# Optimization experiments

Measured on AMD Instinct MI355X. Metric: run time of the kernel, lower is better.

## Reference

```python
import jax, jax.numpy as jnp
import numpy as np

B = 512    # batch
C = 64     # total categorical columns (32 admission + 32 discharge)
N = 32     # graph nodes (one per clinical variable)
V = 100    # categories per column
EMB = 32   # entity embedding dim
HID = 64   # TGCN hidden channels
E = 256    # edges
T = 37     # periods (max LOS)


def setup_inputs() -> dict:
    key = jax.random.key(0)
    ks = jax.random.split(key, 16)

    def lin(k, fi, fo):
        return jax.random.normal(k, (fi, fo), jnp.float32) / np.float32(np.sqrt(fi))

    return {
        "x_batch": jax.random.randint(ks[0], (B, C), 0, V),
        "LOS_batch": jax.random.randint(ks[1], (B,), 0, 38).astype(jnp.int32),
        "template_edge_index": jax.random.randint(ks[2], (2, E), 0, N),
        # per-column entity embedding tables [C, V, EMB]
        "emb_table": jax.random.normal(ks[3], (C, V, EMB), jnp.float32) * 0.05,
        # TGCN gate GCN weights/biases
        "W_z": lin(ks[4], EMB, HID), "b_z": jnp.zeros((HID,), jnp.float32),
        "W_r": lin(ks[5], EMB, HID), "b_r": jnp.zeros((HID,), jnp.float32),
        "W_h": lin(ks[6], EMB, HID), "b_h": jnp.zeros((HID,), jnp.float32),
        # TGCN gate linear layers (input = concat(conv_out, H))
        "L_z": lin(ks[7], 2 * HID, HID), "lb_z": jnp.zeros((HID,), jnp.float32),
        "L_r": lin(ks[8], 2 * HID, HID), "lb_r": jnp.zeros((HID,), jnp.float32),
        "L_h": lin(ks[9], 2 * HID, HID), "lb_h": jnp.zeros((HID,), jnp.float32),
        # A3TGCN temporal attention parameter over periods
        "att": jax.random.uniform(ks[10], (T,), jnp.float32),
        # classifier MLP (num_classes=2 -> out_dim=1)
        "Wc1": lin(ks[11], HID, 2 * HID), "bc1": jnp.zeros((2 * HID,), jnp.float32),
        "Wc2": lin(ks[12], 2 * HID, 1), "bc2": jnp.zeros((1,), jnp.float32),
    }


def reference(x_batch, LOS_batch, template_edge_index, emb_table,
              W_z, b_z, W_r, b_r, W_h, b_h,
              L_z, lb_z, L_r, lb_r, L_h, lb_h,
              att, Wc1, bc1, Wc2, bc2):
    # --- entity embedding: one table per column -> [B, C, EMB]
    x_emb = emb_table[jnp.arange(C)[None, :], x_batch]
    ad, dis = x_emb[:, :N], x_emb[:, N:]              # [B, N, EMB] each

    # --- to_temporal: admission features while t < LOS, discharge after
    mask = jnp.arange(T)[None, None, None, :] < LOS_batch[:, None, None, None]
    x_temporal = jnp.where(mask, ad[..., None], dis[..., None])  # [B,N,EMB,T]

    # --- GCN symmetric normalization with self loops (PyG gcn_norm)
    loops = jnp.arange(N)
    src = jnp.concatenate([template_edge_index[0], loops])
    dst = jnp.concatenate([template_edge_index[1], loops])
    deg = jnp.zeros((N,), x_emb.dtype).at[dst].add(1.0)
    dinv = jnp.where(deg > 0, deg ** -0.5, 0.0)
    norm = dinv[src] * dinv[dst]                      # [E+N]

    def gcn(x, W, b):                                 # x: [B,N,Fin] -> [B,N,HID]
        xw = x @ W
        msg = xw[:, src, :] * norm[None, :, None]
        return jnp.zeros((B, N, W.shape[1]), x.dtype).at[:, dst, :].add(msg) + b

    H0 = jnp.zeros((B, N, HID), x_emb.dtype)          # hidden state (A3TGCN passes H=None each period)

    def tgcn_cell(Xt):                                # Xt: [B,N,EMB]
        Z = jax.nn.sigmoid(jnp.concatenate([gcn(Xt, W_z, b_z), H0], -1) @ L_z + lb_z)
        R = jax.nn.sigmoid(jnp.concatenate([gcn(Xt, W_r, b_r), H0], -1) @ L_r + lb_r)
        Ht = jnp.tanh(jnp.concatenate([gcn(Xt, W_h, b_h), H0 * R], -1) @ L_h + lb_h)
        return Z * H0 + (1.0 - Z) * Ht

    probs = jax.nn.softmax(att)
    Xs = jnp.moveaxis(x_temporal, -1, 0)              # [T,B,N,EMB]

    def step(acc, p_X):
        p, Xt = p_X
        return acc + p * tgcn_cell(Xt), None

    H_accum, _ = jax.lax.scan(step, H0, (probs, Xs))  # [B,N,HID]
    pooled = H_accum.mean(axis=1)                     # [B,HID]
    return jax.nn.relu(pooled @ Wc1 + bc1) @ Wc2 + bc2  # [B,1]
```

## Files before the change

### kernel.cpp

```cpp
#include <hip/hip_runtime.h>
#include <math.h>

#define BATCH 512
#define CCH   64
#define NND   32
#define VOC   100
#define DEMB  32
#define HID   64
#define NEDGE 256
#define NT    37
#define NTH   512

__global__ __launch_bounds__(NTH, 4)
void a3_fused_w8(const int* __restrict__ xbg, const int* __restrict__ LOSb,
                 const int* __restrict__ tei, const float* __restrict__ emb,
                 const float* __restrict__ Wz, const float* __restrict__ bz,
                 const float* __restrict__ Wh, const float* __restrict__ bh,
                 const float* __restrict__ Lz, const float* __restrict__ lbz,
                 const float* __restrict__ Lh, const float* __restrict__ lbh,
                 const float* __restrict__ att,
                 const float* __restrict__ Wc1, const float* __restrict__ bc1,
                 const float* __restrict__ Wc2, const float* __restrict__ bc2,
                 float* __restrict__ out) {
    __shared__ float sA[NND][NND];
    __shared__ float xe[CCH][DEMB];
    __shared__ float xa[CCH][DEMB];
    __shared__ float sWL[2][DEMB][HID];
    __shared__ float scb[2][HID];
    __shared__ float satt[NT];
    __shared__ int   xb[CCH];
    __shared__ int   sdeg[NND];
    __shared__ float sdinv[NND];
    __shared__ float part[8][HID];
    __shared__ float pooled[HID];
    __shared__ float h1s[2 * HID];

    const int b   = blockIdx.x;
    const int tid = threadIdx.x;
    const int hd  = tid & 63;
    const int wv  = tid >> 6;

    if (tid < CCH) xb[tid] = xbg[b * CCH + tid];
    if (tid < NT)  satt[tid] = att[tid];
    if (tid < NND) sdeg[tid] = 1;
#pragma unroll
    for (int i = 0; i < 2; ++i) ((float*)sA)[tid + NTH * i] = 0.f;
    int s_e = 0, d_e = 0;
    if (tid < NEDGE) { s_e = tei[tid]; d_e = tei[NEDGE + tid]; }
    __syncthreads();

    if (tid < NEDGE) atomicAdd(&sdeg[d_e], 1);
#pragma unroll
    for (int i = 0; i < 4; ++i) {
        const int el = tid + NTH * i;
        const int c = el >> 5, k = el & 31;
        xe[c][k] = emb[(c * VOC + xb[c]) * DEMB + k];
    }
    __syncthreads();
    if (tid < NND) sdinv[tid] = rsqrtf((float)sdeg[tid]);
    __syncthreads();
    if (tid < NEDGE) atomicAdd(&sA[d_e][s_e], sdinv[s_e] * sdinv[d_e]);
    if (tid < NND) atomicAdd(&sA[tid][tid], sdinv[tid] * sdinv[tid]);

    {
        float az[4], ah[4];
#pragma unroll
        for (int i = 0; i < 4; ++i) { az[i] = 0.f; ah[i] = 0.f; }
#pragma unroll 4
        for (int k = 0; k < HID; ++k) {
            const float lz = Lz[k * HID + hd];
            const float lh = Lh[k * HID + hd];
#pragma unroll
            for (int i = 0; i < 4; ++i) {
                const int e = wv + 8 * i;
                az[i] = fmaf(Wz[e * HID + k], lz, az[i]);
                ah[i] = fmaf(Wh[e * HID + k], lh, ah[i]);
            }
        }
#pragma unroll
        for (int i = 0; i < 4; ++i) {
            sWL[0][wv + 8 * i][hd] = az[i];
            sWL[1][wv + 8 * i][hd] = ah[i];
        }
    }

    if (tid < 2 * HID) {
        const int g = tid >> 6, c = tid & 63;
        const float* Lg  = g ? Lh  : Lz;
        const float* bg  = g ? bh  : bz;
        const float* lbg = g ? lbh : lbz;
        float s = lbg[c];
#pragma unroll 4
        for (int k = 0; k < HID; ++k) s = fmaf(bg[k], Lg[k * HID + c], s);
        scb[g][c] = s;
    }

    const int los = LOSb[b];
    float cA;
    {
        float m = satt[0];
        for (int t = 1; t < NT; ++t) m = fmaxf(m, satt[t]);
        float tot = 0.f, pre = 0.f;
        for (int t = 0; t < NT; ++t) {
            const float e = __expf(satt[t] - m);
            tot += e;
            if (t < los) pre += e;
        }
        cA = pre / tot;
    }
    const float cD = 1.0f - cA;
    __syncthreads();

#pragma unroll
    for (int i = 0; i < 4; ++i) {
        const int o = tid + NTH * i;
        const int r = o >> 5, k = o & 31;
        const int n = r & 31, vb = r & 32;
        float s = 0.f;
#pragma unroll
        for (int q = 0; q < NND; ++q) s = fmaf(sA[n][q], xe[vb | q][k], s);
        xa[r][k] = s;
    }
    __syncthreads();

    float psum = 0.f;
#pragma unroll
    for (int j = 0; j < 8; ++j) {
        const int r = wv + 8 * j;
        float zl = scb[0][hd], hl = scb[1][hd];
#pragma unroll
        for (int k = 0; k < DEMB; ++k) {
            const float x = xa[r][k];
            zl = fmaf(x, sWL[0][k][hd], zl);
            hl = fmaf(x, sWL[1][k][hd], hl);
        }
        const float Z  = 1.0f / (1.0f + __expf(-zl));
        const float e2 = __expf(2.0f * hl);
        const float Ht = (e2 - 1.0f) / (e2 + 1.0f);
        const float w  = (r < NND) ? cA : cD;
        psum = fmaf(w, (1.0f - Z) * Ht, psum);
    }
    part[wv][hd] = psum;
    __syncthreads();

    if (tid < HID) {
        float s = 0.f;
#pragma unroll
        for (int g = 0; g < 8; ++g) s += part[g][tid];
        pooled[tid] = s * (1.0f / NND);
    }
    __syncthreads();

    if (tid < 2 * HID) {
        float a = bc1[tid];
#pragma unroll 4
        for (int k = 0; k < HID; ++k) a = fmaf(pooled[k], Wc1[k * 2 * HID + tid], a);
        h1s[tid] = fmaxf(a, 0.f) * Wc2[tid];
    }
    __syncthreads();
    if (tid < 64) {
        float v = h1s[tid] + h1s[tid + 64];
#pragma unroll
        for (int off = 32; off; off >>= 1) v += __shfl_down(v, off);
        if (tid == 0) out[b] = v + bc2[0];
    }
}

extern "C" void kernel_launch(void* const* d_in, const int* in_sizes, int n_in,
                              void* d_out, int out_size, void* d_ws, size_t ws_size,
                              hipStream_t stream) {
    const int*   x_batch = (const int*)d_in[0];
    const int*   LOSb    = (const int*)d_in[1];
    const int*   tei     = (const int*)d_in[2];
    const float* emb     = (const float*)d_in[3];
    const float* Wz      = (const float*)d_in[4];
    const float* bz      = (const float*)d_in[5];
    const float* Wh      = (const float*)d_in[8];
    const float* bh      = (const float*)d_in[9];
    const float* Lz      = (const float*)d_in[10];
    const float* lbz     = (const float*)d_in[11];
    const float* Lh      = (const float*)d_in[14];
    const float* lbh     = (const float*)d_in[15];
    const float* att     = (const float*)d_in[16];
    const float* Wc1     = (const float*)d_in[17];
    const float* bc1     = (const float*)d_in[18];
    const float* Wc2     = (const float*)d_in[19];
    const float* bc2     = (const float*)d_in[20];
    float* outp = (float*)d_out;

    hipLaunchKernelGGL(a3_fused_w8, dim3(BATCH), dim3(NTH), 0, stream,
                       x_batch, LOSb, tei, emb, Wz, bz, Wh, bh, Lz, lbz, Lh, lbh,
                       att, Wc1, bc1, Wc2, bc2, outp);
}
```

Baseline: 35.34 us.

## Precompute per-vocabulary projected embeddings in a prep kernel, simplify main kernel

Adds a prep kernel that folds the embedding tables through the combined W·L gate weights, giving a [2, C, V, HID] table of projected rows. It also computes the normalized adjacency, the gate biases and the softmax prefix sums for every LOS value once. The main kernel then gathers projected rows and aggregates them over the graph, which removes the per-batch weight products, the degree computation and the softmax. The cost is a second launch and about 3.3 MB of global writes and gathers.

```diff
diff --git a/kernel.cpp b/kernel.cpp
--- a/kernel.cpp
+++ b/kernel.cpp
@@ -9,28 +9,115 @@
 #define HID   64
 #define NEDGE 256
 #define NT    37
-#define NTH   512
-
-__global__ __launch_bounds__(NTH, 4)
-void a3_fused_w8(const int* __restrict__ xbg, const int* __restrict__ LOSb,
-                 const int* __restrict__ tei, const float* __restrict__ emb,
-                 const float* __restrict__ Wz, const float* __restrict__ bz,
-                 const float* __restrict__ Wh, const float* __restrict__ bh,
-                 const float* __restrict__ Lz, const float* __restrict__ lbz,
-                 const float* __restrict__ Lh, const float* __restrict__ lbh,
-                 const float* __restrict__ att,
-                 const float* __restrict__ Wc1, const float* __restrict__ bc1,
-                 const float* __restrict__ Wc2, const float* __restrict__ bc2,
-                 float* __restrict__ out) {
-    __shared__ float sA[NND][NND];
-    __shared__ float xe[CCH][DEMB];
-    __shared__ float xa[CCH][DEMB];
+
+__device__ float gT[2 * CCH * VOC * HID];
+__device__ float gA[NND * NND];
+__device__ float gCB[2 * HID];
+__device__ float gPC[NT + 1];
+
+__global__ __launch_bounds__(512)
+void a3_prep(const int* __restrict__ tei, const float* __restrict__ att,
+             const float* __restrict__ emb,
+             const float* __restrict__ Wz, const float* __restrict__ bz,
+             const float* __restrict__ Wh, const float* __restrict__ bh,
+             const float* __restrict__ Lz, const float* __restrict__ lbz,
+             const float* __restrict__ Lh, const float* __restrict__ lbh) {
     __shared__ float sWL[2][DEMB][HID];
-    __shared__ float scb[2][HID];
-    __shared__ float satt[NT];
-    __shared__ int   xb[CCH];
     __shared__ int   sdeg[NND];
     __shared__ float sdinv[NND];
+    __shared__ float lA[NND][NND];
+
+    const int tid = threadIdx.x;
+    const int o   = tid & 63;
+    const int wv  = tid >> 6;
+    const int c   = blockIdx.x;
+
+    {
+        float az[4], ah[4];
+#pragma unroll
+        for (int i = 0; i < 4; ++i) { az[i] = 0.f; ah[i] = 0.f; }
+        for (int m = 0; m < HID; ++m) {
+            const float lz = Lz[m * HID + o];
+            const float lh = Lh[m * HID + o];
+#pragma unroll
+            for (int i = 0; i < 4; ++i) {
+                const int k = wv + 8 * i;
+                az[i] = fmaf(Wz[k * HID + m], lz, az[i]);
+                ah[i] = fmaf(Wh[k * HID + m], lh, ah[i]);
+            }
+        }
+#pragma unroll
+        for (int i = 0; i < 4; ++i) {
+            sWL[0][wv + 8 * i][o] = az[i];
+            sWL[1][wv + 8 * i][o] = ah[i];
+        }
+    }
+    __syncthreads();
+
+    for (int vi = 0; vi < 13; ++vi) {
+        const int v = wv + 8 * vi;
+        if (v < VOC) {
+            float tz = 0.f, th = 0.f;
+            for (int k = 0; k < DEMB; ++k) {
+                const float e = emb[(c * VOC + v) * DEMB + k];
+                tz = fmaf(e, sWL[0][k][o], tz);
+                th = fmaf(e, sWL[1][k][o], th);
+            }
+            gT[((0 * CCH + c) * VOC + v) * HID + o] = tz;
+            gT[((1 * CCH + c) * VOC + v) * HID + o] = th;
+        }
+    }
+
+    if (blockIdx.x == 0) {
+        if (tid < NND) sdeg[tid] = 1;
+#pragma unroll
+        for (int i = 0; i < 2; ++i) ((float*)lA)[tid + 512 * i] = 0.f;
+        __syncthreads();
+        int se = 0, de = 0;
+        if (tid < NEDGE) {
+            se = tei[tid]; de = tei[NEDGE + tid];
+            atomicAdd(&sdeg[de], 1);
+        }
+        __syncthreads();
+        if (tid < NND) sdinv[tid] = rsqrtf((float)sdeg[tid]);
+        __syncthreads();
+        if (tid < NEDGE) atomicAdd(&lA[de][se], sdinv[se] * sdinv[de]);
+        if (tid < NND)   atomicAdd(&lA[tid][tid], sdinv[tid] * sdinv[tid]);
+        __syncthreads();
+#pragma unroll
+        for (int i = 0; i < 2; ++i) gA[tid + 512 * i] = ((float*)lA)[tid + 512 * i];
+
+        if (tid < 2 * HID) {
+            const int g = tid >> 6, cc = tid & 63;
+            const float* Lg  = g ? Lh  : Lz;
+            const float* bg  = g ? bh  : bz;
+            const float* lbg = g ? lbh : lbz;
+            float s = lbg[cc];
+            for (int k = 0; k < HID; ++k) s = fmaf(bg[k], Lg[k * HID + cc], s);
+            gCB[tid] = s;
+        }
+        if (tid <= NT) {
+            float m = att[0];
+            for (int t = 1; t < NT; ++t) m = fmaxf(m, att[t]);
+            float tot = 0.f, pre = 0.f;
+            for (int t = 0; t < NT; ++t) {
+                const float e = __expf(att[t] - m);
+                tot += e;
+                if (t < tid) pre += e;
+            }
+            gPC[tid] = pre / tot;
+        }
+    }
+}
+
+__global__ __launch_bounds__(512, 4)
+void a3_main(const int* __restrict__ xbg, const int* __restrict__ LOSb,
+             const float* __restrict__ Wc1, const float* __restrict__ bc1,
+             const float* __restrict__ Wc2, const float* __restrict__ bc2,
+             float* __restrict__ out) {
+    __shared__ float sA[NND][NND];
+    __shared__ int   srb[2][CCH];
+    __shared__ float scb[2][HID];
     __shared__ float part[8][HID];
     __shared__ float pooled[HID];
     __shared__ float h1s[2 * HID];
@@ -40,107 +127,46 @@
     const int hd  = tid & 63;
     const int wv  = tid >> 6;
 
-    if (tid < CCH) xb[tid] = xbg[b * CCH + tid];
-    if (tid < NT)  satt[tid] = att[tid];
-    if (tid < NND) sdeg[tid] = 1;
-#pragma unroll
-    for (int i = 0; i < 2; ++i) ((float*)sA)[tid + NTH * i] = 0.f;
-    int s_e = 0, d_e = 0;
-    if (tid < NEDGE) { s_e = tei[tid]; d_e = tei[NEDGE + tid]; }
-    __syncthreads();
-
-    if (tid < NEDGE) atomicAdd(&sdeg[d_e], 1);
-#pragma unroll
-    for (int i = 0; i < 4; ++i) {
-        const int el = tid + NTH * i;
-        const int c = el >> 5, k = el & 31;
-        xe[c][k] = emb[(c * VOC + xb[c]) * DEMB + k];
-    }
-    __syncthreads();
-    if (tid < NND) sdinv[tid] = rsqrtf((float)sdeg[tid]);
-    __syncthreads();
-    if (tid < NEDGE) atomicAdd(&sA[d_e][s_e], sdinv[s_e] * sdinv[d_e]);
-    if (tid < NND) atomicAdd(&sA[tid][tid], sdinv[tid] * sdinv[tid]);
-
-    {
-        float az[4], ah[4];
-#pragma unroll
-        for (int i = 0; i < 4; ++i) { az[i] = 0.f; ah[i] = 0.f; }
-#pragma unroll 4
-        for (int k = 0; k < HID; ++k) {
-            const float lz = Lz[k * HID + hd];
-            const float lh = Lh[k * HID + hd];
-#pragma unroll
-            for (int i = 0; i < 4; ++i) {
-                const int e = wv + 8 * i;
-                az[i] = fmaf(Wz[e * HID + k], lz, az[i]);
-                ah[i] = fmaf(Wh[e * HID + k], lh, ah[i]);
-            }
-        }
-#pragma unroll
-        for (int i = 0; i < 4; ++i) {
-            sWL[0][wv + 8 * i][hd] = az[i];
-            sWL[1][wv + 8 * i][hd] = ah[i];
-        }
-    }
-
-    if (tid < 2 * HID) {
-        const int g = tid >> 6, c = tid & 63;
-        const float* Lg  = g ? Lh  : Lz;
-        const float* bg  = g ? bh  : bz;
-        const float* lbg = g ? lbh : lbz;
-        float s = lbg[c];
-#pragma unroll 4
-        for (int k = 0; k < HID; ++k) s = fmaf(bg[k], Lg[k * HID + c], s);
-        scb[g][c] = s;
-    }
-
-    const int los = LOSb[b];
-    float cA;
-    {
-        float m = satt[0];
-        for (int t = 1; t < NT; ++t) m = fmaxf(m, satt[t]);
-        float tot = 0.f, pre = 0.f;
-        for (int t = 0; t < NT; ++t) {
-            const float e = __expf(satt[t] - m);
-            tot += e;
-            if (t < los) pre += e;
-        }
-        cA = pre / tot;
-    }
+#pragma unroll
+    for (int i = 0; i < 2; ++i) ((float*)sA)[tid + 512 * i] = gA[tid + 512 * i];
+    if (tid < CCH) {
+        const int xbv = xbg[b * CCH + tid];
+        srb[0][tid] = ((0 * CCH + tid) * VOC + xbv) * HID;
+        srb[1][tid] = ((1 * CCH + tid) * VOC + xbv) * HID;
+    }
+    if (tid < 2 * HID) ((float*)scb)[tid] = gCB[tid];
+    const float cA = gPC[LOSb[b]];
     const float cD = 1.0f - cA;
     __syncthreads();
 
-#pragma unroll
-    for (int i = 0; i < 4; ++i) {
-        const int o = tid + NTH * i;
-        const int r = o >> 5, k = o & 31;
-        const int n = r & 31, vb = r & 32;
-        float s = 0.f;
-#pragma unroll
-        for (int q = 0; q < NND; ++q) s = fmaf(sA[n][q], xe[vb | q][k], s);
-        xa[r][k] = s;
-    }
-    __syncthreads();
-
+    const int var = wv >> 2;
+    const int n0  = (wv & 3) * 8;
+    float zacc[8], hacc[8];
+#pragma unroll
+    for (int j = 0; j < 8; ++j) { zacc[j] = 0.f; hacc[j] = 0.f; }
+    for (int q = 0; q < NND; ++q) {
+        const int cc = var * NND + q;
+        const float tz = gT[srb[0][cc] + hd];
+        const float th = gT[srb[1][cc] + hd];
+#pragma unroll
+        for (int j = 0; j < 8; ++j) {
+            const float a = sA[n0 + j][q];
+            zacc[j] = fmaf(a, tz, zacc[j]);
+            hacc[j] = fmaf(a, th, hacc[j]);
+        }
+    }
+    const float wr = var ? cD : cA;
     float psum = 0.f;
 #pragma unroll
     for (int j = 0; j < 8; ++j) {
-        const int r = wv + 8 * j;
-        float zl = scb[0][hd], hl = scb[1][hd];
-#pragma unroll
-        for (int k = 0; k < DEMB; ++k) {
-            const float x = xa[r][k];
-            zl = fmaf(x, sWL[0][k][hd], zl);
-            hl = fmaf(x, sWL[1][k][hd], hl);
-        }
+        const float zl = zacc[j] + scb[0][hd];
+        const float hl = hacc[j] + scb[1][hd];
         const float Z  = 1.0f / (1.0f + __expf(-zl));
         const float e2 = __expf(2.0f * hl);
         const float Ht = (e2 - 1.0f) / (e2 + 1.0f);
-        const float w  = (r < NND) ? cA : cD;
-        psum = fmaf(w, (1.0f - Z) * Ht, psum);
-    }
-    part[wv][hd] = psum;
+        psum = fmaf(1.0f - Z, Ht, psum);
+    }
+    part[wv][hd] = wr * psum;
     __syncthreads();
 
     if (tid < HID) {
@@ -188,7 +214,8 @@
     const float* bc2     = (const float*)d_in[20];
     float* outp = (float*)d_out;
 
-    hipLaunchKernelGGL(a3_fused_w8, dim3(BATCH), dim3(NTH), 0, stream,
-                       x_batch, LOSb, tei, emb, Wz, bz, Wh, bh, Lz, lbz, Lh, lbh,
-                       att, Wc1, bc1, Wc2, bc2, outp);
+    hipLaunchKernelGGL(a3_prep, dim3(CCH), dim3(512), 0, stream,
+                       tei, att, emb, Wz, bz, Wh, bh, Lz, lbz, Lh, lbh);
+    hipLaunchKernelGGL(a3_main, dim3(BATCH), dim3(512), 0, stream,
+                       x_batch, LOSb, Wc1, bc1, Wc2, bc2, outp);
 }
```

Result: no change. 35.51 us (+0.5%).
